# Optimization experiments

Measured on AMD Instinct MI355X. Metric: run time of the kernel, lower is better.

The kernel has to match this reference:

```python
import jax, jax.numpy as jnp
import numpy as np

NUM_SEGMENTS = 50000


def _mlp(x, W1, b1, W2, b2):
    # hidden layer with ReLU, linear output (num_hidden_lyr=1)
    h = jax.nn.relu(x @ W1 + b1)
    return h @ W2 + b2


def setup_inputs() -> dict:
    key = jax.random.key(0)
    ks = jax.random.split(key, 10)
    N, D = 1000000, 128
    ins = jax.random.normal(ks[0], (N, D), dtype=jnp.float32)
    batch = jnp.sort(jax.random.randint(ks[1], (N,), 0, NUM_SEGMENTS, dtype=jnp.int64))
    s = 1.0 / np.sqrt(D)
    phi_W1 = jax.random.uniform(ks[2], (D, D), jnp.float32, -s, s)
    phi_b1 = jax.random.uniform(ks[3], (D,), jnp.float32, -s, s)
    phi_W2 = jax.random.uniform(ks[4], (D, D), jnp.float32, -s, s)
    phi_b2 = jax.random.uniform(ks[5], (D,), jnp.float32, -s, s)
    rho_W1 = jax.random.uniform(ks[6], (D, D), jnp.float32, -s, s)
    rho_b1 = jax.random.uniform(ks[7], (D,), jnp.float32, -s, s)
    rho_W2 = jax.random.uniform(ks[8], (D, D), jnp.float32, -s, s)
    rho_b2 = jax.random.uniform(ks[9], (D,), jnp.float32, -s, s)
    return {"ins": ins, "batch": batch, "dim": 0,
            "phi_W1": phi_W1, "phi_b1": phi_b1, "phi_W2": phi_W2, "phi_b2": phi_b2,
            "rho_W1": rho_W1, "rho_b1": rho_b1, "rho_W2": rho_W2, "rho_b2": rho_b2}


def reference(ins, batch, dim, phi_W1, phi_b1, phi_W2, phi_b2, rho_W1, rho_b1, rho_W2, rho_b2):
    # dim is always 0 in this usage (scatter over set elements)
    h = _mlp(ins, phi_W1, phi_b1, phi_W2, phi_b2)          # [N, out_dim]
    seg_sum = jax.ops.segment_sum(h, batch, num_segments=NUM_SEGMENTS)  # [B, out_dim]
    counts = jax.ops.segment_sum(jnp.ones((h.shape[0],), h.dtype), batch,
                                 num_segments=NUM_SEGMENTS)
    seg_mean = seg_sum / jnp.maximum(counts, 1.0)[:, None]  # scatter_mean semantics
    return _mlp(seg_mean, rho_W1, rho_b1, rho_W2, rho_b2)   # [B, out_dim]
```

## Files before the change

### kernel.cpp

```cpp
#include <hip/hip_runtime.h>
#include <hip/hip_fp16.h>

typedef _Float16 f16;
typedef __attribute__((ext_vector_type(8))) _Float16 f16x8;
typedef __attribute__((ext_vector_type(4))) _Float16 f16x4;
typedef __attribute__((ext_vector_type(4))) float f32x4;

#define NSEG 50000
#define DIM 128
#define LDST 136

#define MFMA16(a, b, c) __builtin_amdgcn_mfma_f32_16x16x32_f16((a), (b), (c), 0, 0, 0)

__global__ void zero_kernel(float4* __restrict__ p, int n4) {
    int i = blockIdx.x * blockDim.x + threadIdx.x;
    if (i < n4) p[i] = make_float4(0.f, 0.f, 0.f, 0.f);
}

__global__ void prepack_kernel(const float* __restrict__ w0, const float* __restrict__ w1,
                               const float* __restrict__ w2, const float* __restrict__ w3,
                               f16* __restrict__ packs) {
    int gid = blockIdx.x * blockDim.x + threadIdx.x;
    int q = gid >> 11;
    int r = gid & 2047;
    int tm = r >> 8;
    int kt = (r >> 6) & 3;
    int lane = r & 63;
    const float* W = (q == 0) ? w0 : (q == 1) ? w1 : (q == 2) ? w2 : w3;
    int mp = tm * 16 + (lane & 15);
    int kb = kt * 32 + ((lane >> 4) & 3) * 8;
    f16* dst = packs + q * 16384 + ((size_t)((tm * 4 + kt) * 64 + lane)) * 8;
#pragma unroll
    for (int j = 0; j < 8; ++j)
        dst[j] = (f16)W[(size_t)(kb + j) * DIM + mp];
}

__global__ __launch_bounds__(256, 2)
void phi_scatter_kernel(const float* __restrict__ x, const int* __restrict__ batch,
                        const f16* __restrict__ pack1, const f16* __restrict__ pack2,
                        const float* __restrict__ b1, const float* __restrict__ b2,
                        float* __restrict__ seg_sum, float* __restrict__ counts, int N) {
    __shared__ f16 buf[128 * LDST];
    __shared__ int seg_s[128];

    int tid = threadIdx.x;
    int wave = tid >> 6, lane = tid & 63, g = lane >> 4, ln = lane & 15;
    long long r0 = (long long)blockIdx.x * 128;
    int nvalid = min(128, N - (int)r0);

#pragma unroll
    for (int i = 0; i < 16; ++i) {
        int flat = i * 1024 + tid * 4;
        int row = flat >> 7, col = flat & 127;
        float4 v = make_float4(0.f, 0.f, 0.f, 0.f);
        if (row < nvalid) v = *(const float4*)(x + (r0 + row) * DIM + col);
        f16x4 h;
        h[0] = (f16)v.x; h[1] = (f16)v.y; h[2] = (f16)v.z; h[3] = (f16)v.w;
        *(f16x4*)(buf + row * LDST + col) = h;
    }
    if (tid < 128) {
        int s = 0;
        if (tid < nvalid) {
            s = batch[r0 + tid];
            s = (s < 0) ? 0 : ((s >= NSEG) ? NSEG - 1 : s);
        } else {
            s = -1;
        }
        seg_s[tid] = s;
    }
    __syncthreads();

    int tm0 = wave * 2;
    f32x4 acc[2][8];
#pragma unroll
    for (int a = 0; a < 2; ++a)
#pragma unroll
        for (int t = 0; t < 8; ++t) acc[a][t] = (f32x4){0.f, 0.f, 0.f, 0.f};

#pragma unroll
    for (int kt = 0; kt < 4; ++kt) {
        f16x8 a0 = *(const f16x8*)(pack1 + ((size_t)((tm0 + 0) * 4 + kt) * 64 + lane) * 8);
        f16x8 a1 = *(const f16x8*)(pack1 + ((size_t)((tm0 + 1) * 4 + kt) * 64 + lane) * 8);
#pragma unroll
        for (int tn = 0; tn < 8; ++tn) {
            f16x8 b = *(const f16x8*)(buf + (tn * 16 + ln) * LDST + kt * 32 + g * 8);
            acc[0][tn] = MFMA16(a0, b, acc[0][tn]);
            acc[1][tn] = MFMA16(a1, b, acc[1][tn]);
        }
    }
    __syncthreads();

#pragma unroll
    for (int a = 0; a < 2; ++a) {
        int tm = tm0 + a;
        float4 bv = *(const float4*)(b1 + tm * 16 + g * 4);
#pragma unroll
        for (int tn = 0; tn < 8; ++tn) {
            f32x4 c = acc[a][tn];
            f16x4 h;
            h[0] = (f16)fmaxf(c[0] + bv.x, 0.f);
            h[1] = (f16)fmaxf(c[1] + bv.y, 0.f);
            h[2] = (f16)fmaxf(c[2] + bv.z, 0.f);
            h[3] = (f16)fmaxf(c[3] + bv.w, 0.f);
            *(f16x4*)(buf + (tn * 16 + ln) * LDST + tm * 16 + g * 4) = h;
        }
    }
    __syncthreads();

#pragma unroll
    for (int a = 0; a < 2; ++a)
#pragma unroll
        for (int t = 0; t < 8; ++t) acc[a][t] = (f32x4){0.f, 0.f, 0.f, 0.f};
#pragma unroll
    for (int kt = 0; kt < 4; ++kt) {
        f16x8 a0 = *(const f16x8*)(pack2 + ((size_t)((tm0 + 0) * 4 + kt) * 64 + lane) * 8);
        f16x8 a1 = *(const f16x8*)(pack2 + ((size_t)((tm0 + 1) * 4 + kt) * 64 + lane) * 8);
#pragma unroll
        for (int tn = 0; tn < 8; ++tn) {
            f16x8 b = *(const f16x8*)(buf + (tn * 16 + ln) * LDST + kt * 32 + g * 8);
            acc[0][tn] = MFMA16(a0, b, acc[0][tn]);
            acc[1][tn] = MFMA16(a1, b, acc[1][tn]);
        }
    }
    __syncthreads();

#pragma unroll
    for (int a = 0; a < 2; ++a) {
        int tm = tm0 + a;
        float4 bv = *(const float4*)(b2 + tm * 16 + g * 4);
#pragma unroll
        for (int tn = 0; tn < 8; ++tn) {
            f32x4 c = acc[a][tn];
            f16x4 h;
            h[0] = (f16)(c[0] + bv.x);
            h[1] = (f16)(c[1] + bv.y);
            h[2] = (f16)(c[2] + bv.z);
            h[3] = (f16)(c[3] + bv.w);
            *(f16x4*)(buf + (tn * 16 + ln) * LDST + tm * 16 + g * 4) = h;
        }
    }
    __syncthreads();

    int n = tid & 127, half = tid >> 7;
    int m0 = half * 64, m1 = min(m0 + 64, nvalid);
    if (m0 < m1) {
        float accv = 0.f, cnt = 0.f;
        int cur = seg_s[m0];
        for (int m = m0; m < m1; ++m) {
            int s = seg_s[m];
            float v = (float)buf[m * LDST + n];
            if (s != cur) {
                atomicAdd(seg_sum + (size_t)cur * DIM + n, accv);
                if (n == 0) atomicAdd(counts + cur, cnt);
                accv = 0.f; cnt = 0.f; cur = s;
            }
            accv += v; cnt += 1.f;
        }
        atomicAdd(seg_sum + (size_t)cur * DIM + n, accv);
        if (n == 0) atomicAdd(counts + cur, cnt);
    }
}

__global__ __launch_bounds__(256, 2)
void rho_kernel(const float* __restrict__ seg_sum, const float* __restrict__ counts,
                const f16* __restrict__ pack1, const f16* __restrict__ pack2,
                const float* __restrict__ b1, const float* __restrict__ b2,
                float* __restrict__ out) {
    __shared__ f16 buf[128 * LDST];

    int tid = threadIdx.x;
    int wave = tid >> 6, lane = tid & 63, g = lane >> 4, ln = lane & 15;
    int s0 = blockIdx.x * 128;
    int nvalid = min(128, NSEG - s0);

#pragma unroll
    for (int i = 0; i < 16; ++i) {
        int flat = i * 1024 + tid * 4;
        int row = flat >> 7, col = flat & 127;
        float4 v = make_float4(0.f, 0.f, 0.f, 0.f);
        if (row < nvalid) {
            v = *(const float4*)(seg_sum + (size_t)(s0 + row) * DIM + col);
            float inv = 1.f / fmaxf(counts[s0 + row], 1.f);
            v.x *= inv; v.y *= inv; v.z *= inv; v.w *= inv;
        }
        f16x4 h;
        h[0] = (f16)v.x; h[1] = (f16)v.y; h[2] = (f16)v.z; h[3] = (f16)v.w;
        *(f16x4*)(buf + row * LDST + col) = h;
    }
    __syncthreads();

    int tm0 = wave * 2;
    f32x4 acc[2][8];
#pragma unroll
    for (int a = 0; a < 2; ++a)
#pragma unroll
        for (int t = 0; t < 8; ++t) acc[a][t] = (f32x4){0.f, 0.f, 0.f, 0.f};

#pragma unroll
    for (int kt = 0; kt < 4; ++kt) {
        f16x8 a0 = *(const f16x8*)(pack1 + ((size_t)((tm0 + 0) * 4 + kt) * 64 + lane) * 8);
        f16x8 a1 = *(const f16x8*)(pack1 + ((size_t)((tm0 + 1) * 4 + kt) * 64 + lane) * 8);
#pragma unroll
        for (int tn = 0; tn < 8; ++tn) {
            f16x8 b = *(const f16x8*)(buf + (tn * 16 + ln) * LDST + kt * 32 + g * 8);
            acc[0][tn] = MFMA16(a0, b, acc[0][tn]);
            acc[1][tn] = MFMA16(a1, b, acc[1][tn]);
        }
    }
    __syncthreads();

#pragma unroll
    for (int a = 0; a < 2; ++a) {
        int tm = tm0 + a;
        float4 bv = *(const float4*)(b1 + tm * 16 + g * 4);
#pragma unroll
        for (int tn = 0; tn < 8; ++tn) {
            f32x4 c = acc[a][tn];
            f16x4 h;
            h[0] = (f16)fmaxf(c[0] + bv.x, 0.f);
            h[1] = (f16)fmaxf(c[1] + bv.y, 0.f);
            h[2] = (f16)fmaxf(c[2] + bv.z, 0.f);
            h[3] = (f16)fmaxf(c[3] + bv.w, 0.f);
            *(f16x4*)(buf + (tn * 16 + ln) * LDST + tm * 16 + g * 4) = h;
        }
    }
    __syncthreads();

#pragma unroll
    for (int a = 0; a < 2; ++a)
#pragma unroll
        for (int t = 0; t < 8; ++t) acc[a][t] = (f32x4){0.f, 0.f, 0.f, 0.f};
#pragma unroll
    for (int kt = 0; kt < 4; ++kt) {
        f16x8 a0 = *(const f16x8*)(pack2 + ((size_t)((tm0 + 0) * 4 + kt) * 64 + lane) * 8);
        f16x8 a1 = *(const f16x8*)(pack2 + ((size_t)((tm0 + 1) * 4 + kt) * 64 + lane) * 8);
#pragma unroll
        for (int tn = 0; tn < 8; ++tn) {
            f16x8 b = *(const f16x8*)(buf + (tn * 16 + ln) * LDST + kt * 32 + g * 8);
            acc[0][tn] = MFMA16(a0, b, acc[0][tn]);
            acc[1][tn] = MFMA16(a1, b, acc[1][tn]);
        }
    }

#pragma unroll
    for (int a = 0; a < 2; ++a) {
        int tm = tm0 + a;
        float4 bv = *(const float4*)(b2 + tm * 16 + g * 4);
#pragma unroll
        for (int tn = 0; tn < 8; ++tn) {
            int srow = tn * 16 + ln;
            if (s0 + srow < NSEG) {
                f32x4 c = acc[a][tn];
                float4 o = make_float4(c[0] + bv.x, c[1] + bv.y, c[2] + bv.z, c[3] + bv.w);
                *(float4*)(out + (size_t)(s0 + srow) * DIM + tm * 16 + g * 4) = o;
            }
        }
    }
}

extern "C" void kernel_launch(void* const* d_in, const int* in_sizes, int n_in,
                              void* d_out, int out_size, void* d_ws, size_t ws_size,
                              hipStream_t stream) {
    const float* ins = (const float*)d_in[0];
    const int* batch = (const int*)d_in[1];
    const float* phi_W1 = (const float*)d_in[3];
    const float* phi_b1 = (const float*)d_in[4];
    const float* phi_W2 = (const float*)d_in[5];
    const float* phi_b2 = (const float*)d_in[6];
    const float* rho_W1 = (const float*)d_in[7];
    const float* rho_b1 = (const float*)d_in[8];
    const float* rho_W2 = (const float*)d_in[9];
    const float* rho_b2 = (const float*)d_in[10];

    int N = in_sizes[0] / DIM;

    float* seg_sum = (float*)d_out;
    char* ws = (char*)d_ws;
    float* counts = (float*)ws;
    f16*   packs  = (f16*)(ws + 200704);

    zero_kernel<<<(NSEG * DIM / 4 + 255) / 256, 256, 0, stream>>>((float4*)seg_sum, NSEG * DIM / 4);
    zero_kernel<<<(NSEG / 4 + 255) / 256, 256, 0, stream>>>((float4*)counts, NSEG / 4);

    prepack_kernel<<<32, 256, 0, stream>>>(phi_W1, phi_W2, rho_W1, rho_W2, packs);

    int nblk = (N + 127) / 128;
    phi_scatter_kernel<<<nblk, 256, 0, stream>>>(ins, batch, packs, packs + 16384,
                                                 phi_b1, phi_b2, seg_sum, counts, N);

    rho_kernel<<<(NSEG + 127) / 128, 256, 0, stream>>>(seg_sum, counts,
                                                       packs + 2 * 16384, packs + 3 * 16384,
                                                       rho_b1, rho_b2, (float*)d_out);
}
```

Before: 781.8 us.

## Fuse zero kernels, raise occupancy, batch scatter loads, halve rho tile rows

Merges the two zeroing launches into one kernel. Raises launch bounds to 4 waves-per-EU hints for the phi and rho kernels. Rewrites the segmented reduction loop to load eight rows of segment ids and values at a time and skip invalid rows via a negative-id sentinel. Shrinks the rho tile to 64 rows so more blocks run concurrently. The tighter register budget may cause spills in the phi kernel, and the unrolled scatter loop now relies on seg_s holding -1 for padding rows, which must be set in the elided code.

```diff
diff --git a/kernel.cpp b/kernel.cpp
--- a/kernel.cpp
+++ b/kernel.cpp
@@ -12,9 +12,16 @@
 
 #define MFMA16(a, b, c) __builtin_amdgcn_mfma_f32_16x16x32_f16((a), (b), (c), 0, 0, 0)
 
-__global__ void zero_kernel(float4* __restrict__ p, int n4) {
+__global__ void zero2_kernel(float4* __restrict__ a, int n4a,
+                             float4* __restrict__ b, int n4b) {
     int i = blockIdx.x * blockDim.x + threadIdx.x;
-    if (i < n4) p[i] = make_float4(0.f, 0.f, 0.f, 0.f);
+    float4 z = make_float4(0.f, 0.f, 0.f, 0.f);
+    if (i < n4a) {
+        a[i] = z;
+    } else {
+        int j = i - n4a;
+        if (j < n4b) b[j] = z;
+    }
 }
 
 __global__ void prepack_kernel(const float* __restrict__ w0, const float* __restrict__ w1,
@@ -35,7 +42,7 @@
         dst[j] = (f16)W[(size_t)(kb + j) * DIM + mp];
 }
 
-__global__ __launch_bounds__(256, 2)
+__global__ __launch_bounds__(256, 4)
 void phi_scatter_kernel(const float* __restrict__ x, const int* __restrict__ batch,
                         const f16* __restrict__ pack1, const f16* __restrict__ pack2,
                         const float* __restrict__ b1, const float* __restrict__ b2,
@@ -142,39 +149,52 @@
     __syncthreads();
 
     int n = tid & 127, half = tid >> 7;
-    int m0 = half * 64, m1 = min(m0 + 64, nvalid);
-    if (m0 < m1) {
-        float accv = 0.f, cnt = 0.f;
-        int cur = seg_s[m0];
-        for (int m = m0; m < m1; ++m) {
-            int s = seg_s[m];
-            float v = (float)buf[m * LDST + n];
-            if (s != cur) {
-                atomicAdd(seg_sum + (size_t)cur * DIM + n, accv);
-                if (n == 0) atomicAdd(counts + cur, cnt);
-                accv = 0.f; cnt = 0.f; cur = s;
+    int m0 = half * 64;
+    float accv = 0.f, cnt = 0.f;
+    int cur = seg_s[m0];
+#pragma unroll
+    for (int grp = 0; grp < 8; ++grp) {
+        float v[8];
+        int s[8];
+#pragma unroll
+        for (int j = 0; j < 8; ++j) {
+            int m = m0 + grp * 8 + j;
+            s[j] = seg_s[m];
+            v[j] = (float)buf[m * LDST + n];
+        }
+#pragma unroll
+        for (int j = 0; j < 8; ++j) {
+            if (s[j] != cur) {
+                if (cur >= 0) {
+                    atomicAdd(seg_sum + (size_t)cur * DIM + n, accv);
+                    if (n == 0) atomicAdd(counts + cur, cnt);
+                }
+                accv = 0.f; cnt = 0.f; cur = s[j];
             }
-            accv += v; cnt += 1.f;
-        }
+            accv += v[j]; cnt += 1.f;
+        }
+    }
+    if (cur >= 0) {
         atomicAdd(seg_sum + (size_t)cur * DIM + n, accv);
         if (n == 0) atomicAdd(counts + cur, cnt);
     }
 }
 
-__global__ __launch_bounds__(256, 2)
+#define RROWS 64
+__global__ __launch_bounds__(256, 4)
 void rho_kernel(const float* __restrict__ seg_sum, const float* __restrict__ counts,
                 const f16* __restrict__ pack1, const f16* __restrict__ pack2,
                 const float* __restrict__ b1, const float* __restrict__ b2,
                 float* __restrict__ out) {
-    __shared__ f16 buf[128 * LDST];
+    __shared__ f16 buf[RROWS * LDST];
 
     int tid = threadIdx.x;
     int wave = tid >> 6, lane = tid & 63, g = lane >> 4, ln = lane & 15;
-    int s0 = blockIdx.x * 128;
-    int nvalid = min(128, NSEG - s0);
-
-#pragma unroll
-    for (int i = 0; i < 16; ++i) {
+    int s0 = blockIdx.x * RROWS;
+    int nvalid = min(RROWS, NSEG - s0);
+
+#pragma unroll
+    for (int i = 0; i < 8; ++i) {
         int flat = i * 1024 + tid * 4;
         int row = flat >> 7, col = flat & 127;
         float4 v = make_float4(0.f, 0.f, 0.f, 0.f);
@@ -190,18 +210,18 @@
     __syncthreads();
 
     int tm0 = wave * 2;
-    f32x4 acc[2][8];
+    f32x4 acc[2][4];
 #pragma unroll
     for (int a = 0; a < 2; ++a)
 #pragma unroll
-        for (int t = 0; t < 8; ++t) acc[a][t] = (f32x4){0.f, 0.f, 0.f, 0.f};
+        for (int t = 0; t < 4; ++t) acc[a][t] = (f32x4){0.f, 0.f, 0.f, 0.f};
 
 #pragma unroll
     for (int kt = 0; kt < 4; ++kt) {
         f16x8 a0 = *(const f16x8*)(pack1 + ((size_t)((tm0 + 0) * 4 + kt) * 64 + lane) * 8);
         f16x8 a1 = *(const f16x8*)(pack1 + ((size_t)((tm0 + 1) * 4 + kt) * 64 + lane) * 8);
 #pragma unroll
-        for (int tn = 0; tn < 8; ++tn) {
+        for (int tn = 0; tn < 4; ++tn) {
             f16x8 b = *(const f16x8*)(buf + (tn * 16 + ln) * LDST + kt * 32 + g * 8);
             acc[0][tn] = MFMA16(a0, b, acc[0][tn]);
             acc[1][tn] = MFMA16(a1, b, acc[1][tn]);
@@ -214,7 +234,7 @@
         int tm = tm0 + a;
         float4 bv = *(const float4*)(b1 + tm * 16 + g * 4);
 #pragma unroll
-        for (int tn = 0; tn < 8; ++tn) {
+        for (int tn = 0; tn < 4; ++tn) {
             f32x4 c = acc[a][tn];
             f16x4 h;
             h[0] = (f16)fmaxf(c[0] + bv.x, 0.f);
@@ -229,13 +249,13 @@
 #pragma unroll
     for (int a = 0; a < 2; ++a)
 #pragma unroll
-        for (int t = 0; t < 8; ++t) acc[a][t] = (f32x4){0.f, 0.f, 0.f, 0.f};
+        for (int t = 0; t < 4; ++t) acc[a][t] = (f32x4){0.f, 0.f, 0.f, 0.f};
 #pragma unroll
     for (int kt = 0; kt < 4; ++kt) {
         f16x8 a0 = *(const f16x8*)(pack2 + ((size_t)((tm0 + 0) * 4 + kt) * 64 + lane) * 8);
         f16x8 a1 = *(const f16x8*)(pack2 + ((size_t)((tm0 + 1) * 4 + kt) * 64 + lane) * 8);
 #pragma unroll
-        for (int tn = 0; tn < 8; ++tn) {
+        for (int tn = 0; tn < 4; ++tn) {
             f16x8 b = *(const f16x8*)(buf + (tn * 16 + ln) * LDST + kt * 32 + g * 8);
             acc[0][tn] = MFMA16(a0, b, acc[0][tn]);
             acc[1][tn] = MFMA16(a1, b, acc[1][tn]);
@@ -247,7 +267,7 @@
         int tm = tm0 + a;
         float4 bv = *(const float4*)(b2 + tm * 16 + g * 4);
 #pragma unroll
-        for (int tn = 0; tn < 8; ++tn) {
+        for (int tn = 0; tn < 4; ++tn) {
             int srow = tn * 16 + ln;
             if (s0 + srow < NSEG) {
                 f32x4 c = acc[a][tn];
@@ -279,8 +299,10 @@
     float* counts = (float*)ws;
     f16*   packs  = (f16*)(ws + 200704);
 
-    zero_kernel<<<(NSEG * DIM / 4 + 255) / 256, 256, 0, stream>>>((float4*)seg_sum, NSEG * DIM / 4);
-    zero_kernel<<<(NSEG / 4 + 255) / 256, 256, 0, stream>>>((float4*)counts, NSEG / 4);
+    int n4a = NSEG * DIM / 4;
+    int n4b = NSEG / 4;
+    zero2_kernel<<<(n4a + n4b + 255) / 256, 256, 0, stream>>>((float4*)seg_sum, n4a,
+                                                              (float4*)counts, n4b);
 
     prepack_kernel<<<32, 256, 0, stream>>>(phi_W1, phi_W2, rho_W1, rho_W2, packs);
 
@@ -288,7 +310,7 @@
     phi_scatter_kernel<<<nblk, 256, 0, stream>>>(ins, batch, packs, packs + 16384,
                                                  phi_b1, phi_b2, seg_sum, counts, N);
 
-    rho_kernel<<<(NSEG + 127) / 128, 256, 0, stream>>>(seg_sum, counts,
+    rho_kernel<<<(NSEG + RROWS - 1) / RROWS, 256, 0, stream>>>(seg_sum, counts,
                                                        packs + 2 * 16384, packs + 3 * 16384,
                                                        rho_b1, rho_b2, (float*)d_out);
 }
```

Result: faster. 766.2 us (-2.0%).
